# Optimization experiments

Hardware: AMD Instinct MI355X
Metric: run time of the kernel (lower is better)

The kernel has to match this reference:

```python
import jax, jax.numpy as jnp
import numpy as np

B, T, I, H, L = 32, 512, 1024, 1024, 2

def setup_inputs() -> dict:
    key = jax.random.key(0)
    ks = jax.random.split(key, 5)
    x = jax.random.normal(ks[0], (B, T, I), dtype=jnp.float32)
    # nn.Linear weight layout: [out_features, in_features] = [4H, in+H]
    scale0 = (6.0 / (4 * H + I + H)) ** 0.5  # xavier uniform bound
    scale1 = (6.0 / (4 * H + H + H)) ** 0.5
    W0 = jax.random.uniform(ks[1], (4 * H, I + H), minval=-scale0, maxval=scale0, dtype=jnp.float32)
    W1 = jax.random.uniform(ks[2], (4 * H, H + H), minval=-scale1, maxval=scale1, dtype=jnp.float32)
    # bias: zeros, with forget-gate slice (first H) set to 1, per reset_parameters
    b = jnp.zeros((4 * H,), dtype=jnp.float32).at[:H].set(1.0)
    return {"x": x, "W0": W0, "b0": b, "W1": W1, "b1": b}

def _cell(x_in, h_prev, c_prev, W, b):
    # combined:[B, in+H] @ W.T -> [B, 4H]
    gates = jnp.concatenate([x_in, h_prev], axis=1) @ W.T + b
    f, i, g, o = jnp.split(gates, 4, axis=1)
    f = jax.nn.sigmoid(f)
    i = jax.nn.sigmoid(i)
    g = jnp.tanh(g)
    o = jax.nn.sigmoid(o)
    c_next = f * c_prev + i * g
    h_next = o * jnp.tanh(c_next)
    return h_next, c_next

def reference(x, W0, b0, W1, b1):
    Ws = (W0, W1)
    bs = (b0, b1)
    x_t_major = jnp.transpose(x, (1, 0, 2))  # [T, B, I]
    h0 = jnp.zeros((L, B, H), dtype=x.dtype)
    c0 = jnp.zeros((L, B, H), dtype=x.dtype)

    def step(carry, x_t):
        h, c = carry
        inp = x_t
        hs, cs = [], []
        for l in range(L):
            h_new, c_new = _cell(inp, h[l], c[l], Ws[l], bs[l])
            hs.append(h_new)
            cs.append(c_new)
            inp = h_new  # dropout=0 -> identity between layers
        return (jnp.stack(hs), jnp.stack(cs)), inp

    (h_n, c_n), outs = jax.lax.scan(step, (h0, c0), x_t_major)
    outputs = jnp.transpose(outs, (1, 0, 2))  # batch_first
    return outputs, h_n, c_n
```

## Files before the change

### kernel.cpp

```cpp
#include <hip/hip_runtime.h>
#include <hip/hip_bf16.h>
#include <cstdint>
#include <cstddef>


typedef unsigned short ush;
typedef short bf16x8 __attribute__((ext_vector_type(8)));
typedef float f32x4 __attribute__((ext_vector_type(4)));
typedef int i32x4 __attribute__((ext_vector_type(4)));
typedef unsigned long long u64;

#define TT 512
#define NA 64
#define RING 8

__device__ __forceinline__ ush f2bf(float f) {
  __hip_bfloat16 h = __float2bfloat16(f);
  return *reinterpret_cast<ush*>(&h);
}
__device__ __forceinline__ float sigm(float x) { return 1.f / (1.f + __expf(-x)); }

__device__ __forceinline__ unsigned int aload(const unsigned int* p) {
  return __hip_atomic_load(p, __ATOMIC_RELAXED, __HIP_MEMORY_SCOPE_AGENT);
}
__device__ __forceinline__ void astore(unsigned int* p, unsigned int v) {
  __hip_atomic_store(p, v, __ATOMIC_RELAXED, __HIP_MEMORY_SCOPE_AGENT);
}
__device__ __forceinline__ float afload(const float* p) {
  return __hip_atomic_load(p, __ATOMIC_RELAXED, __HIP_MEMORY_SCOPE_AGENT);
}

__global__ __launch_bounds__(256) void cast_w1k(const float* __restrict__ W,
                                                ush* __restrict__ Wb, int off) {
  int j = blockIdx.x;
  int k = threadIdx.x * 4;
  float4 v = *(const float4*)(W + (size_t)j * 2048 + off + k);
  ushort4 o;
  o.x = f2bf(v.x); o.y = f2bf(v.y); o.z = f2bf(v.z); o.w = f2bf(v.w);
  *(ushort4*)(Wb + (size_t)j * 1024 + k) = o;
}

__global__ __launch_bounds__(256) void swzW(const float* __restrict__ W,
                                            ush* __restrict__ D, int coloff) {
  int n = blockIdx.x * 256 + threadIdx.x;
  int lane = n & 63, ch = (n >> 6) & 15, w = (n >> 10) & 7, i = n >> 13;
  int l15 = lane & 15, quad = lane >> 4, g = w & 3, kh = w >> 2;
  int row = g * 1024 + i * 16 + l15;
  int col = coloff + kh * 512 + ch * 32 + quad * 8;
  const float* src = W + (size_t)row * 2048 + col;
  float4 v0 = ((const float4*)src)[0];
  float4 v1 = ((const float4*)src)[1];
  ushort4 o0, o1;
  o0.x = f2bf(v0.x); o0.y = f2bf(v0.y); o0.z = f2bf(v0.z); o0.w = f2bf(v0.w);
  o1.x = f2bf(v1.x); o1.y = f2bf(v1.y); o1.z = f2bf(v1.z); o1.w = f2bf(v1.w);
  *(ushort4*)(D + (size_t)n * 8) = o0;
  *(ushort4*)(D + (size_t)n * 8 + 4) = o1;
}

__global__ __launch_bounds__(256) void swz1h(const float* __restrict__ W,
                                             ush* __restrict__ D) {
  int n = blockIdx.x * 256 + threadIdx.x;
  int lane = n & 63, ch = (n >> 6) & 7, w = (n >> 9) & 7, jb = n >> 12;
  int l15 = lane & 15, quad = lane >> 4, rh = w & 1, kq = w >> 1;
  int r32 = rh * 16 + l15;
  int row = (r32 >> 3) * 1024 + jb * 8 + (r32 & 7);
  int col = 1024 + kq * 256 + ch * 32 + quad * 8;
  const float* src = W + (size_t)row * 2048 + col;
  float4 v0 = ((const float4*)src)[0];
  float4 v1 = ((const float4*)src)[1];
  ushort4 o0, o1;
  o0.x = f2bf(v0.x); o0.y = f2bf(v0.y); o0.z = f2bf(v0.z); o0.w = f2bf(v0.w);
  o1.x = f2bf(v1.x); o1.y = f2bf(v1.y); o1.z = f2bf(v1.z); o1.w = f2bf(v1.w);
  *(ushort4*)(D + (size_t)n * 8) = o0;
  *(ushort4*)(D + (size_t)n * 8 + 4) = o1;
}

__global__ __launch_bounds__(256) void zeroreg(uint4* __restrict__ p) {
  p[blockIdx.x * 256 + threadIdx.x] = uint4{0, 0, 0, 0};
}

__global__ __launch_bounds__(256) void gemm128(
    const float* __restrict__ xA, const ush* __restrict__ Wb,
    const float* __restrict__ bias, float* __restrict__ G, int t0) {
  __shared__ ush As[128][88];
  __shared__ ush Bs[128][88];
  int tid = threadIdx.x;
  int bn = blockIdx.x, bm = blockIdx.y;
  int srow = tid >> 1;
  int shalf = (tid & 1) * 32;
  int lane = tid & 63, quad = lane >> 4, l15 = lane & 15;
  int w = tid >> 6;
  int m_base = (w >> 1) * 64, n_base = (w & 1) * 64;

  int r = bm * 128 + srow;
  const float* axf = xA + ((size_t)(r & 31) * TT + t0 + (r >> 5)) * 1024;
  const ush* wrow = Wb + (size_t)(bn * 128 + srow) * 1024;

  f32x4 acc[4][4];
#pragma unroll
  for (int i = 0; i < 4; ++i)
#pragma unroll
    for (int j = 0; j < 4; ++j) acc[i][j] = f32x4{0.f, 0.f, 0.f, 0.f};

  for (int k0 = 0; k0 < 1024; k0 += 64) {
    {
      const float* p = axf + k0 + shalf;
      ush* d = &As[srow][shalf];
#pragma unroll
      for (int s = 0; s < 8; ++s) {
        float4 v = ((const float4*)p)[s];
        ushort4 o;
        o.x = f2bf(v.x); o.y = f2bf(v.y); o.z = f2bf(v.z); o.w = f2bf(v.w);
        ((ushort4*)d)[s] = o;
      }
    }
    {
      const uint4* p = (const uint4*)(wrow + k0 + shalf);
      uint4* d = (uint4*)&Bs[srow][shalf];
#pragma unroll
      for (int s = 0; s < 4; ++s) d[s] = p[s];
    }
    __syncthreads();
#pragma unroll
    for (int kc = 0; kc < 2; ++kc) {
      bf16x8 af[4], bf_[4];
#pragma unroll
      for (int i = 0; i < 4; ++i)
        af[i] = *(const bf16x8*)&As[m_base + i * 16 + l15][kc * 32 + quad * 8];
#pragma unroll
      for (int j = 0; j < 4; ++j)
        bf_[j] = *(const bf16x8*)&Bs[n_base + j * 16 + l15][kc * 32 + quad * 8];
#pragma unroll
      for (int i = 0; i < 4; ++i)
#pragma unroll
        for (int j = 0; j < 4; ++j)
          acc[i][j] = __builtin_amdgcn_mfma_f32_16x16x32_bf16(af[i], bf_[j],
                                                              acc[i][j], 0, 0, 0);
    }
    __syncthreads();
  }

#pragma unroll
  for (int j = 0; j < 4; ++j) {
    int col = bn * 128 + n_base + j * 16 + l15;
    float bj = bias[col];
#pragma unroll
    for (int i = 0; i < 4; ++i) {
      int row = bm * 128 + m_base + i * 16 + quad * 4;
#pragma unroll
      for (int reg = 0; reg < 4; ++reg)
        G[(size_t)(row + reg) * 4096 + col] = acc[i][j][reg] + bj;
    }
  }
}

__global__ __launch_bounds__(512, 2) void lstm_persist(
    const float* __restrict__ G0, const ush* __restrict__ Wsw0,
    const ush* __restrict__ WswP, const ush* __restrict__ Wsw1h,
    const float* __restrict__ b1,
    ush* __restrict__ h0r, ush* __restrict__ h1r, float* __restrict__ Pr,
    unsigned int* __restrict__ flg,
    float* __restrict__ cst, float* __restrict__ OUT,
    float* __restrict__ hno, float* __restrict__ cno,
    int t0, int Tc, int last) {
  __shared__ ush hbuf[32768];
  __shared__ float pg[8][32][20];
  char* hb = (char*)hbuf;

  int tid = threadIdx.x;
  int bid = blockIdx.x;
  int w = tid >> 6, lane = tid & 63, quad = lane >> 4, l15 = lane & 15;
  unsigned int* prog0 = flg;
  unsigned int* prog1 = flg + 1024;
  unsigned int* progP = flg + 3072;

  if (bid < NA) {
    int c0 = bid * 16;
    const ush* wp = Wsw0 + ((size_t)bid * 8 + w) * 8192 + (size_t)lane * 8;
    bf16x8 wreg[16];
#pragma unroll
    for (int ch = 0; ch < 16; ++ch) wreg[ch] = *(const bf16x8*)(wp + ch * 512);
#pragma unroll
    for (int ch = 0; ch < 16; ++ch) asm volatile("" : "+v"(wreg[ch]));
    int b = tid >> 4, c = tid & 15;
    int ci = b * 1024 + c0 + c;
    float creg = (t0 > 0) ? cst[ci] : 0.f;
    int mPc = t0;
    int kbase = (w >> 2) * 1024 + quad * 16;
    int x0 = (l15 & 7) << 4;
    const char* a0p = hb + l15 * 2048;
    const char* a1p = hb + (16 + l15) * 2048;

    for (int s = 0; s < Tc; ++s) {
      int t = t0 + s;
      const float* grow = G0 + (size_t)(s * 32 + b) * 4096 + c0 + c;
      float g0v = grow[0], g1v = grow[1024], g2v = grow[2048], g3v = grow[3072];
      if (w == 0) {
        if ((int)aload(&prog0[lane * 16]) < t) {
          do { __builtin_amdgcn_s_sleep(1); } while ((int)aload(&prog0[lane * 16]) < t);
        }
        while (mPc < t - (RING - 1)) {
          int m = (int)aload(&progP[lane * 16]);
#pragma unroll
          for (int d = 1; d < 64; d <<= 1) m = min(m, __shfl_xor(m, d));
          mPc = m;
          if (mPc < t - (RING - 1)) __builtin_amdgcn_s_sleep(2);
        }
      }
      __syncthreads();
      {
        const char* src = (const char*)h0r + (size_t)((t - 1) & (RING - 1)) * 65536;
        i32x4 r_[8];
#pragma unroll
        for (int s2 = 0; s2 < 8; ++s2) {
          int gi = s2 * 512 + tid;
          asm volatile("global_load_dwordx4 %0, %1, off sc1"
                       : "=v"(r_[s2]) : "v"(src + (size_t)gi * 16));
        }
        asm volatile("s_waitcnt vmcnt(0)" ::: "memory");
        __builtin_amdgcn_sched_barrier(0);
#pragma unroll
        for (int s2 = 0; s2 < 8; ++s2) {
          int gi = s2 * 512 + tid;
          int r = gi >> 7, kb = (gi & 127) * 16;
          *(i32x4*)(hb + r * 2048 + (kb ^ ((r & 7) << 4))) = r_[s2];
        }
      }
      __syncthreads();
      f32x4 acc0 = {0.f, 0.f, 0.f, 0.f}, acc1 = {0.f, 0.f, 0.f, 0.f};
#pragma unroll
      for (int ch = 0; ch < 16; ++ch) {
        int kb = kbase + ch * 64;
        bf16x8 a0 = *(const bf16x8*)(a0p + (kb ^ x0));
        bf16x8 a1 = *(const bf16x8*)(a1p + (kb ^ x0));
        acc0 = __builtin_amdgcn_mfma_f32_16x16x32_bf16(a0, wreg[ch], acc0, 0, 0, 0);
        acc1 = __builtin_amdgcn_mfma_f32_16x16x32_bf16(a1, wreg[ch], acc1, 0, 0, 0);
      }
#pragma unroll
      for (int reg = 0; reg < 4; ++reg) {
        pg[w][quad * 4 + reg][l15] = acc0[reg];
        pg[w][16 + quad * 4 + reg][l15] = acc1[reg];
      }
      __syncthreads();
      float s0 = g0v + pg[0][b][c] + pg[4][b][c];
      float s1 = g1v + pg[1][b][c] + pg[5][b][c];
      float s2 = g2v + pg[2][b][c] + pg[6][b][c];
      float s3 = g3v + pg[3][b][c] + pg[7][b][c];
      float fg = sigm(s0), ig = sigm(s1), gv = tanhf(s2), og = sigm(s3);
      creg = fg * creg + ig * gv;
      float hnv = og * tanhf(creg);
      float ho = __shfl_xor(hnv, 1);
      unsigned int pk = (unsigned int)f2bf(hnv) | ((unsigned int)f2bf(ho) << 16);
      unsigned int pk2 = __shfl_xor(pk, 2);
      u64 d0 = (u64)pk | ((u64)pk2 << 32);
      u64 d1 = (u64)__shfl_xor((long long)d0, 4);
      if ((tid & 7) == 0) {
        i32x4 v;
        v.x = (int)d0; v.y = (int)(d0 >> 32);
        v.z = (int)d1; v.w = (int)(d1 >> 32);
        char* dp = (char*)(h0r + (size_t)(t & (RING - 1)) * 32768 +
                           (size_t)b * 1024 + c0 + c);
        asm volatile("global_store_dwordx4 %0, %1, off sc1"
                     :: "v"(dp), "v"(v) : "memory");
      }
      if (t == TT - 1) hno[ci] = hnv;
      asm volatile("s_waitcnt vmcnt(0)" ::: "memory");
      __syncthreads();
      if (tid == 0) astore(&prog0[bid * 16], (unsigned int)(t + 1));
    }
    cst[ci] = creg;
    if (last) cno[ci] = creg;
  } else if (bid < 2 * NA) {
    int p = bid - NA;
    int c0 = p * 16;
    const ush* wp = WswP + ((size_t)p * 8 + w) * 8192 + (size_t)lane * 8;
    bf16x8 wreg[16];
#pragma unroll
    for (int ch = 0; ch < 16; ++ch) wreg[ch] = *(const bf16x8*)(wp + ch * 512);
#pragma unroll
    for (int ch = 0; ch < 16; ++ch) asm volatile("" : "+v"(wreg[ch]));
    int b = tid >> 4, c = tid & 15;
    int m1c = t0;
    int kbase = (w >> 2) * 1024 + quad * 16;
    int x0 = (l15 & 7) << 4;
    const char* a0p = hb + l15 * 2048;
    const char* a1p = hb + (16 + l15) * 2048;

    for (int s = 0; s < Tc; ++s) {
      int t = t0 + s;
      if (w == 0) {
        if ((int)aload(&prog0[lane * 16]) < t + 1) {
          do { __builtin_amdgcn_s_sleep(1); } while ((int)aload(&prog0[lane * 16]) < t + 1);
        }
        while (m1c < t - (RING - 1)) {
          int m = (int)aload(&prog1[lane * 16]);
          m = min(m, (int)aload(&prog1[(64 + lane) * 16]));
#pragma unroll
          for (int d = 1; d < 64; d <<= 1) m = min(m, __shfl_xor(m, d));
          m1c = m;
          if (m1c < t - (RING - 1)) __builtin_amdgcn_s_sleep(2);
        }
      }
      __syncthreads();
      {
        const char* src = (const char*)h0r + (size_t)(t & (RING - 1)) * 65536;
        i32x4 r_[8];
#pragma unroll
        for (int s2 = 0; s2 < 8; ++s2) {
          int gi = s2 * 512 + tid;
          asm volatile("global_load_dwordx4 %0, %1, off sc1"
                       : "=v"(r_[s2]) : "v"(src + (size_t)gi * 16));
        }
        asm volatile("s_waitcnt vmcnt(0)" ::: "memory");
        __builtin_amdgcn_sched_barrier(0);
#pragma unroll
        for (int s2 = 0; s2 < 8; ++s2) {
          int gi = s2 * 512 + tid;
          int r = gi >> 7, kb = (gi & 127) * 16;
          *(i32x4*)(hb + r * 2048 + (kb ^ ((r & 7) << 4))) = r_[s2];
        }
      }
      __syncthreads();
      f32x4 acc0 = {0.f, 0.f, 0.f, 0.f}, acc1 = {0.f, 0.f, 0.f, 0.f};
#pragma unroll
      for (int ch = 0; ch < 16; ++ch) {
        int kb = kbase + ch * 64;
        bf16x8 a0 = *(const bf16x8*)(a0p + (kb ^ x0));
        bf16x8 a1 = *(const bf16x8*)(a1p + (kb ^ x0));
        acc0 = __builtin_amdgcn_mfma_f32_16x16x32_bf16(a0, wreg[ch], acc0, 0, 0, 0);
        acc1 = __builtin_amdgcn_mfma_f32_16x16x32_bf16(a1, wreg[ch], acc1, 0, 0, 0);
      }
#pragma unroll
      for (int reg = 0; reg < 4; ++reg) {
        pg[w][quad * 4 + reg][l15] = acc0[reg];
        pg[w][16 + quad * 4 + reg][l15] = acc1[reg];
      }
      __syncthreads();
      float s0 = pg[0][b][c] + pg[4][b][c];
      float s1 = pg[1][b][c] + pg[5][b][c];
      float s2 = pg[2][b][c] + pg[6][b][c];
      float s3 = pg[3][b][c] + pg[7][b][c];
      {
        i32x4 v;
        v.x = __float_as_int(s0); v.y = __float_as_int(s1);
        v.z = __float_as_int(s2); v.w = __float_as_int(s3);
        char* dp = (char*)Pr + (size_t)(t & (RING - 1)) * 524288 +
                   (size_t)(b * 1024 + c0 + c) * 16;
        asm volatile("global_store_dwordx4 %0, %1, off sc1"
                     :: "v"(dp), "v"(v) : "memory");
      }
      asm volatile("s_waitcnt vmcnt(0)" ::: "memory");
      __syncthreads();
      if (tid == 0) astore(&progP[p * 16], (unsigned int)(t + 1));
    }
  } else {
    int jb = bid - 2 * NA;
    int c0b = jb * 8;
    const ush* wp = Wsw1h + ((size_t)jb * 8 + w) * 4096 + (size_t)lane * 8;
    bf16x8 wreg[8];
#pragma unroll
    for (int ch = 0; ch < 8; ++ch) wreg[ch] = *(const bf16x8*)(wp + ch * 512);
#pragma unroll
    for (int ch = 0; ch < 8; ++ch) asm volatile("" : "+v"(wreg[ch]));
    bool pw = tid < 256;
    int b = tid >> 3, cc = tid & 7;
    int ci = b * 1024 + c0b + cc;
    float creg = 0.f;
    float biasr[4] = {0.f, 0.f, 0.f, 0.f};
    if (pw) {
      creg = (t0 > 0) ? cst[32768 + ci] : 0.f;
#pragma unroll
      for (int g = 0; g < 4; ++g) biasr[g] = b1[g * 1024 + c0b + cc];
    }
    int kq = w >> 1;
    int kbase = kq * 512 + quad * 16;
    int x0 = (l15 & 7) << 4;
    const char* a0p = hb + l15 * 2048;
    const char* a1p = hb + (16 + l15) * 2048;

    for (int s = 0; s < Tc; ++s) {
      int t = t0 + s;
      if (w == 0) {
        if ((int)aload(&progP[(jb >> 1) * 16]) < t + 1) {
          do { __builtin_amdgcn_s_sleep(1); } while ((int)aload(&progP[(jb >> 1) * 16]) < t + 1);
        }
      }
      __syncthreads();
      float pf[4] = {0.f, 0.f, 0.f, 0.f};
      if (pw) {
        const float* pp = (const float*)((const char*)Pr +
                          (size_t)(t & (RING - 1)) * 524288) +
                          (size_t)(b * 1024 + c0b + cc) * 4;
#pragma unroll
        for (int g = 0; g < 4; ++g) pf[g] = afload(pp + g);
      }
      if (w == 0) {
        while ((int)aload(&prog1[lane * 16]) < t ||
               (int)aload(&prog1[(64 + lane) * 16]) < t)
          __builtin_amdgcn_s_sleep(1);
      }
      __syncthreads();
      {
        const char* src = (const char*)h1r + (size_t)((t - 1) & (RING - 1)) * 65536;
        i32x4 r1_[8];
#pragma unroll
        for (int s2 = 0; s2 < 8; ++s2) {
          int gi = s2 * 512 + tid;
          asm volatile("global_load_dwordx4 %0, %1, off sc1"
                       : "=v"(r1_[s2]) : "v"(src + (size_t)gi * 16));
        }
        asm volatile("s_waitcnt vmcnt(0)" ::: "memory");
        __builtin_amdgcn_sched_barrier(0);
#pragma unroll
        for (int s2 = 0; s2 < 8; ++s2) {
          int gi = s2 * 512 + tid;
          int r = gi >> 7, kb = (gi & 127) * 16;
          *(i32x4*)(hb + r * 2048 + (kb ^ ((r & 7) << 4))) = r1_[s2];
        }
      }
      __syncthreads();
      f32x4 acc0 = {0.f, 0.f, 0.f, 0.f}, acc1 = {0.f, 0.f, 0.f, 0.f};
#pragma unroll
      for (int ch = 0; ch < 8; ++ch) {
        int kb = kbase + ch * 64;
        bf16x8 a0 = *(const bf16x8*)(a0p + (kb ^ x0));
        bf16x8 a1 = *(const bf16x8*)(a1p + (kb ^ x0));
        acc0 = __builtin_amdgcn_mfma_f32_16x16x32_bf16(a0, wreg[ch], acc0, 0, 0, 0);
        acc1 = __builtin_amdgcn_mfma_f32_16x16x32_bf16(a1, wreg[ch], acc1, 0, 0, 0);
      }
#pragma unroll
      for (int reg = 0; reg < 4; ++reg) {
        pg[w][quad * 4 + reg][l15] = acc0[reg];
        pg[w][16 + quad * 4 + reg][l15] = acc1[reg];
      }
      __syncthreads();
      float hnv = 0.f;
      if (pw) {
        float sg[4];
#pragma unroll
        for (int g = 0; g < 4; ++g) {
          int r = g * 8 + cc, rrh = r >> 4, ri = r & 15;
          sg[g] = biasr[g] + pf[g] + pg[rrh][b][ri] + pg[2 + rrh][b][ri] +
                  pg[4 + rrh][b][ri] + pg[6 + rrh][b][ri];
        }
        float fg = sigm(sg[0]), ig = sigm(sg[1]), gv = tanhf(sg[2]),
              og = sigm(sg[3]);
        creg = fg * creg + ig * gv;
        hnv = og * tanhf(creg);
        float ho = __shfl_xor(hnv, 1);
        unsigned int pk = (unsigned int)f2bf(hnv) | ((unsigned int)f2bf(ho) << 16);
        unsigned int pk2 = __shfl_xor(pk, 2);
        u64 d0 = (u64)pk | ((u64)pk2 << 32);
        u64 d1 = (u64)__shfl_xor((long long)d0, 4);
        if ((tid & 7) == 0) {
          i32x4 v;
          v.x = (int)d0; v.y = (int)(d0 >> 32);
          v.z = (int)d1; v.w = (int)(d1 >> 32);
          char* dp = (char*)(h1r + (size_t)(t & (RING - 1)) * 32768 +
                             (size_t)b * 1024 + c0b);
          asm volatile("global_store_dwordx4 %0, %1, off sc1"
                       :: "v"(dp), "v"(v) : "memory");
        }
      }
      asm volatile("s_waitcnt vmcnt(0)" ::: "memory");
      __syncthreads();
      if (tid == 0) astore(&prog1[jb * 16], (unsigned int)(t + 1));
      if (pw) {
        OUT[((size_t)b * TT + t) * 1024 + c0b + cc] = hnv;
        if (t == TT - 1) hno[32768 + ci] = hnv;
      }
    }
    if (pw) {
      cst[32768 + ci] = creg;
      if (last) cno[32768 + ci] = creg;
    }
  }
}

extern "C" void kernel_launch(void* const* d_in, const int* in_sizes, int n_in,
                              void* d_out, int out_size, void* d_ws, size_t ws_size,
                              hipStream_t stream) {
  const float* x = (const float*)d_in[0];
  const float* W0 = (const float*)d_in[1];
  const float* b0 = (const float*)d_in[2];
  const float* W1 = (const float*)d_in[3];
  const float* b1 = (const float*)d_in[4];
  float* OUT = (float*)d_out;

  int Tc = 4;
  {
    const int cand[8] = {512, 256, 128, 64, 32, 16, 8, 4};
    for (int i = 0; i < 8; ++i) {
      size_t need = 39075840ull + (size_t)cand[i] * 524288;
      if (need <= ws_size) { Tc = cand[i]; break; }
    }
  }
  char* ws = (char*)d_ws;
  ush* Wxb0 = (ush*)ws;
  ush* Wsw0 = (ush*)(ws + 8388608);
  ush* WswP = (ush*)(ws + 16777216);
  ush* Wsw1h = (ush*)(ws + 25165824);
  ush* h0r = (ush*)(ws + 33554432);
  ush* h1r = (ush*)(ws + 34078720);
  float* Pr = (float*)(ws + 34603008);
  unsigned int* flg = (unsigned int*)(ws + 38797312);
  float* cst = (float*)(ws + 38813696);
  float* G = (float*)(ws + 39075840);

  cast_w1k<<<4096, 256, 0, stream>>>(W0, Wxb0, 0);
  swzW<<<2048, 256, 0, stream>>>(W0, Wsw0, 1024);
  swzW<<<2048, 256, 0, stream>>>(W1, WswP, 0);
  swz1h<<<2048, 256, 0, stream>>>(W1, Wsw1h);
  zeroreg<<<1284, 256, 0, stream>>>((uint4*)(ws + 33554432));

  float* hnp = OUT + 16777216;
  float* cnp = OUT + 16777216 + 65536;
  dim3 ggrid(32, (unsigned)(Tc * 32 / 128));

  const int NCH = TT / Tc;
  for (int ch = 0; ch < NCH; ++ch) {
    int t0v = ch * Tc;
    int lastv = (ch == NCH - 1) ? 1 : 0;
    gemm128<<<ggrid, 256, 0, stream>>>(x, Wxb0, b0, G, t0v);
    void* pargs[16] = {(void*)&G,     (void*)&Wsw0, (void*)&WswP,
                       (void*)&Wsw1h, (void*)&b1,   (void*)&h0r,
                       (void*)&h1r,   (void*)&Pr,   (void*)&flg,
                       (void*)&cst,   (void*)&OUT,  (void*)&hnp,
                       (void*)&cnp,   (void*)&t0v,  (void*)&Tc,
                       (void*)&lastv};
    hipLaunchCooperativeKernel((void*)lstm_persist, dim3(4 * NA), dim3(512),
                               pargs, 0, stream);
  }
}
```

Before: 2.683 ms.

## Repartition layer-1 recurrent work to 32 blocks with full-K per wave

Layer-1 recurrent blocks drop from 128 to 32. Each wave now covers the full 1024-wide K dimension for 4 hidden columns across all four gates, so the cross-wave LDS reduction and its extra barrier are removed. Gate values are regrouped with in-register shuffles, and the P partials are read with two vector loads. This shrinks the grid and the number of progress flags polled. The cost is longer serial MFMA chains per wave and 32 weight vector registers per lane, which may cut occupancy and add per-step latency on the recurrent critical path.

```diff
diff --git a/kernel.cpp b/kernel.cpp
--- a/kernel.cpp
+++ b/kernel.cpp
@@ -8,6 +8,7 @@
 typedef short bf16x8 __attribute__((ext_vector_type(8)));
 typedef float f32x4 __attribute__((ext_vector_type(4)));
 typedef int i32x4 __attribute__((ext_vector_type(4)));
+typedef int i32x2 __attribute__((ext_vector_type(2)));
 typedef unsigned long long u64;
 
 #define TT 512
@@ -25,9 +26,6 @@
 }
 __device__ __forceinline__ void astore(unsigned int* p, unsigned int v) {
   __hip_atomic_store(p, v, __ATOMIC_RELAXED, __HIP_MEMORY_SCOPE_AGENT);
-}
-__device__ __forceinline__ float afload(const float* p) {
-  return __hip_atomic_load(p, __ATOMIC_RELAXED, __HIP_MEMORY_SCOPE_AGENT);
 }
 
 __global__ __launch_bounds__(256) void cast_w1k(const float* __restrict__ W,
@@ -57,14 +55,13 @@
   *(ushort4*)(D + (size_t)n * 8 + 4) = o1;
 }
 
-__global__ __launch_bounds__(256) void swz1h(const float* __restrict__ W,
+__global__ __launch_bounds__(256) void swz1n(const float* __restrict__ W,
                                              ush* __restrict__ D) {
   int n = blockIdx.x * 256 + threadIdx.x;
-  int lane = n & 63, ch = (n >> 6) & 7, w = (n >> 9) & 7, jb = n >> 12;
-  int l15 = lane & 15, quad = lane >> 4, rh = w & 1, kq = w >> 1;
-  int r32 = rh * 16 + l15;
-  int row = (r32 >> 3) * 1024 + jb * 8 + (r32 & 7);
-  int col = 1024 + kq * 256 + ch * 32 + quad * 8;
+  int lane = n & 63, ch = (n >> 6) & 31, w = (n >> 11) & 7, jb = n >> 14;
+  int l15 = lane & 15, quad = lane >> 4;
+  int row = (l15 >> 2) * 1024 + jb * 32 + w * 4 + (l15 & 3);
+  int col = 1024 + ch * 32 + quad * 8;
   const float* src = W + (size_t)row * 2048 + col;
   float4 v0 = ((const float4*)src)[0];
   float4 v1 = ((const float4*)src)[1];
@@ -156,7 +153,7 @@
 
 __global__ __launch_bounds__(512, 2) void lstm_persist(
     const float* __restrict__ G0, const ush* __restrict__ Wsw0,
-    const ush* __restrict__ WswP, const ush* __restrict__ Wsw1h,
+    const ush* __restrict__ WswP, const ush* __restrict__ Wsw1n,
     const float* __restrict__ b1,
     ush* __restrict__ h0r, ush* __restrict__ h1r, float* __restrict__ Pr,
     unsigned int* __restrict__ flg,
@@ -293,8 +290,7 @@
           do { __builtin_amdgcn_s_sleep(1); } while ((int)aload(&prog0[lane * 16]) < t + 1);
         }
         while (m1c < t - (RING - 1)) {
-          int m = (int)aload(&prog1[lane * 16]);
-          m = min(m, (int)aload(&prog1[(64 + lane) * 16]));
+          int m = (lane < 32) ? (int)aload(&prog1[lane * 16]) : 0x7fffffff;
 #pragma unroll
           for (int d = 1; d < 64; d <<= 1) m = min(m, __shfl_xor(m, d));
           m1c = m;
@@ -355,25 +351,22 @@
     }
   } else {
     int jb = bid - 2 * NA;
-    int c0b = jb * 8;
-    const ush* wp = Wsw1h + ((size_t)jb * 8 + w) * 4096 + (size_t)lane * 8;
-    bf16x8 wreg[8];
-#pragma unroll
-    for (int ch = 0; ch < 8; ++ch) wreg[ch] = *(const bf16x8*)(wp + ch * 512);
-#pragma unroll
-    for (int ch = 0; ch < 8; ++ch) asm volatile("" : "+v"(wreg[ch]));
-    bool pw = tid < 256;
-    int b = tid >> 3, cc = tid & 7;
-    int ci = b * 1024 + c0b + cc;
-    float creg = 0.f;
-    float biasr[4] = {0.f, 0.f, 0.f, 0.f};
-    if (pw) {
-      creg = (t0 > 0) ? cst[32768 + ci] : 0.f;
-#pragma unroll
-      for (int g = 0; g < 4; ++g) biasr[g] = b1[g * 1024 + c0b + cc];
-    }
-    int kq = w >> 1;
-    int kbase = kq * 512 + quad * 16;
+    int c0b = jb * 32;
+    const ush* wp = Wsw1n + (size_t)(jb * 8 + w) * 16384 + (size_t)lane * 8;
+    bf16x8 wreg[32];
+#pragma unroll
+    for (int ch = 0; ch < 32; ++ch) wreg[ch] = *(const bf16x8*)(wp + ch * 512);
+#pragma unroll
+    for (int ch = 0; ch < 32; ++ch) asm volatile("" : "+v"(wreg[ch]));
+    int cl = l15 & 3, bq = (l15 >> 2) & 3;
+    int col = c0b + w * 4 + cl;
+    int ba0 = quad * 4 + bq, ba1 = 16 + quad * 4 + bq;
+    int ci0 = ba0 * 1024 + col, ci1 = ba1 * 1024 + col;
+    float creg0 = (t0 > 0) ? cst[32768 + ci0] : 0.f;
+    float creg1 = (t0 > 0) ? cst[32768 + ci1] : 0.f;
+    float biasr[4];
+#pragma unroll
+    for (int g = 0; g < 4; ++g) biasr[g] = b1[g * 1024 + col];
     int x0 = (l15 & 7) << 4;
     const char* a0p = hb + l15 * 2048;
     const char* a1p = hb + (16 + l15) * 2048;
@@ -381,25 +374,24 @@
     for (int s = 0; s < Tc; ++s) {
       int t = t0 + s;
       if (w == 0) {
-        if ((int)aload(&progP[(jb >> 1) * 16]) < t + 1) {
-          do { __builtin_amdgcn_s_sleep(1); } while ((int)aload(&progP[(jb >> 1) * 16]) < t + 1);
-        }
-      }
-      __syncthreads();
-      float pf[4] = {0.f, 0.f, 0.f, 0.f};
-      if (pw) {
-        const float* pp = (const float*)((const char*)Pr +
-                          (size_t)(t & (RING - 1)) * 524288) +
-                          (size_t)(b * 1024 + c0b + cc) * 4;
-#pragma unroll
-        for (int g = 0; g < 4; ++g) pf[g] = afload(pp + g);
-      }
-      if (w == 0) {
-        while ((int)aload(&prog1[lane * 16]) < t ||
-               (int)aload(&prog1[(64 + lane) * 16]) < t)
-          __builtin_amdgcn_s_sleep(1);
-      }
-      __syncthreads();
+        if (lane < 2) {
+          while ((int)aload(&progP[(2 * jb + lane) * 16]) < t + 1)
+            __builtin_amdgcn_s_sleep(1);
+        }
+        if (lane < 32) {
+          while ((int)aload(&prog1[lane * 16]) < t)
+            __builtin_amdgcn_s_sleep(1);
+        }
+      }
+      __syncthreads();
+      i32x4 pf0, pf1;
+      {
+        const char* pps = (const char*)Pr + (size_t)(t & (RING - 1)) * 524288;
+        asm volatile("global_load_dwordx4 %0, %1, off sc1"
+                     : "=v"(pf0) : "v"(pps + (size_t)ci0 * 16));
+        asm volatile("global_load_dwordx4 %0, %1, off sc1"
+                     : "=v"(pf1) : "v"(pps + (size_t)ci1 * 16));
+      }
       {
         const char* src = (const char*)h1r + (size_t)((t - 1) & (RING - 1)) * 65536;
         i32x4 r1_[8];
@@ -421,59 +413,76 @@
       __syncthreads();
       f32x4 acc0 = {0.f, 0.f, 0.f, 0.f}, acc1 = {0.f, 0.f, 0.f, 0.f};
 #pragma unroll
-      for (int ch = 0; ch < 8; ++ch) {
-        int kb = kbase + ch * 64;
+      for (int ch = 0; ch < 32; ++ch) {
+        int kb = ch * 64 + quad * 16;
         bf16x8 a0 = *(const bf16x8*)(a0p + (kb ^ x0));
         bf16x8 a1 = *(const bf16x8*)(a1p + (kb ^ x0));
         acc0 = __builtin_amdgcn_mfma_f32_16x16x32_bf16(a0, wreg[ch], acc0, 0, 0, 0);
         acc1 = __builtin_amdgcn_mfma_f32_16x16x32_bf16(a1, wreg[ch], acc1, 0, 0, 0);
       }
-#pragma unroll
-      for (int reg = 0; reg < 4; ++reg) {
-        pg[w][quad * 4 + reg][l15] = acc0[reg];
-        pg[w][16 + quad * 4 + reg][l15] = acc1[reg];
-      }
-      __syncthreads();
-      float hnv = 0.f;
-      if (pw) {
-        float sg[4];
-#pragma unroll
-        for (int g = 0; g < 4; ++g) {
-          int r = g * 8 + cc, rrh = r >> 4, ri = r & 15;
-          sg[g] = biasr[g] + pf[g] + pg[rrh][b][ri] + pg[2 + rrh][b][ri] +
-                  pg[4 + rrh][b][ri] + pg[6 + rrh][b][ri];
-        }
-        float fg = sigm(sg[0]), ig = sigm(sg[1]), gv = tanhf(sg[2]),
-              og = sigm(sg[3]);
-        creg = fg * creg + ig * gv;
-        hnv = og * tanhf(creg);
-        float ho = __shfl_xor(hnv, 1);
-        unsigned int pk = (unsigned int)f2bf(hnv) | ((unsigned int)f2bf(ho) << 16);
-        unsigned int pk2 = __shfl_xor(pk, 2);
-        u64 d0 = (u64)pk | ((u64)pk2 << 32);
-        u64 d1 = (u64)__shfl_xor((long long)d0, 4);
-        if ((tid & 7) == 0) {
-          i32x4 v;
-          v.x = (int)d0; v.y = (int)(d0 >> 32);
-          v.z = (int)d1; v.w = (int)(d1 >> 32);
-          char* dp = (char*)(h1r + (size_t)(t & (RING - 1)) * 32768 +
-                             (size_t)b * 1024 + c0b);
-          asm volatile("global_store_dwordx4 %0, %1, off sc1"
-                       :: "v"(dp), "v"(v) : "memory");
-        }
+      {
+        float t0_, t1_, r0_, r1_;
+        if ((bq & 1) == 0) { t0_ = acc0[1]; t1_ = acc0[3]; }
+        else               { t0_ = acc0[0]; t1_ = acc0[2]; }
+        r0_ = __shfl_xor(t0_, 4); r1_ = __shfl_xor(t1_, 4);
+        if ((bq & 1) == 0) { acc0[1] = r0_; acc0[3] = r1_; }
+        else               { acc0[0] = r0_; acc0[2] = r1_; }
+        if ((bq & 2) == 0) { t0_ = acc0[2]; t1_ = acc0[3]; }
+        else               { t0_ = acc0[0]; t1_ = acc0[1]; }
+        r0_ = __shfl_xor(t0_, 8); r1_ = __shfl_xor(t1_, 8);
+        if ((bq & 2) == 0) { acc0[2] = r0_; acc0[3] = r1_; }
+        else               { acc0[0] = r0_; acc0[1] = r1_; }
+        if ((bq & 1) == 0) { t0_ = acc1[1]; t1_ = acc1[3]; }
+        else               { t0_ = acc1[0]; t1_ = acc1[2]; }
+        r0_ = __shfl_xor(t0_, 4); r1_ = __shfl_xor(t1_, 4);
+        if ((bq & 1) == 0) { acc1[1] = r0_; acc1[3] = r1_; }
+        else               { acc1[0] = r0_; acc1[2] = r1_; }
+        if ((bq & 2) == 0) { t0_ = acc1[2]; t1_ = acc1[3]; }
+        else               { t0_ = acc1[0]; t1_ = acc1[1]; }
+        r0_ = __shfl_xor(t0_, 8); r1_ = __shfl_xor(t1_, 8);
+        if ((bq & 2) == 0) { acc1[2] = r0_; acc1[3] = r1_; }
+        else               { acc1[0] = r0_; acc1[1] = r1_; }
+      }
+      float s00 = acc0[0] + __int_as_float(pf0[0]) + biasr[0];
+      float s01 = acc0[1] + __int_as_float(pf0[1]) + biasr[1];
+      float s02 = acc0[2] + __int_as_float(pf0[2]) + biasr[2];
+      float s03 = acc0[3] + __int_as_float(pf0[3]) + biasr[3];
+      float s10 = acc1[0] + __int_as_float(pf1[0]) + biasr[0];
+      float s11 = acc1[1] + __int_as_float(pf1[1]) + biasr[1];
+      float s12 = acc1[2] + __int_as_float(pf1[2]) + biasr[2];
+      float s13 = acc1[3] + __int_as_float(pf1[3]) + biasr[3];
+      float fg0 = sigm(s00), ig0 = sigm(s01), gg0 = tanhf(s02), og0 = sigm(s03);
+      float fg1 = sigm(s10), ig1 = sigm(s11), gg1 = tanhf(s12), og1 = sigm(s13);
+      creg0 = fg0 * creg0 + ig0 * gg0;
+      creg1 = fg1 * creg1 + ig1 * gg1;
+      float h0v = og0 * tanhf(creg0);
+      float h1v = og1 * tanhf(creg1);
+      unsigned pkA = (unsigned)f2bf(h0v) | ((unsigned)f2bf(__shfl_xor(h0v, 1)) << 16);
+      unsigned pkAb = __shfl_xor(pkA, 2);
+      unsigned pkB = (unsigned)f2bf(h1v) | ((unsigned)f2bf(__shfl_xor(h1v, 1)) << 16);
+      unsigned pkBb = __shfl_xor(pkB, 2);
+      if (cl == 0) {
+        i32x2 vA; vA[0] = (int)pkA; vA[1] = (int)pkAb;
+        char* dpA = (char*)(h1r + (size_t)(t & (RING - 1)) * 32768 +
+                            (size_t)ba0 * 1024 + col);
+        asm volatile("global_store_dwordx2 %0, %1, off sc1"
+                     :: "v"(dpA), "v"(vA) : "memory");
+        i32x2 vB; vB[0] = (int)pkB; vB[1] = (int)pkBb;
+        char* dpB = (char*)(h1r + (size_t)(t & (RING - 1)) * 32768 +
+                            (size_t)ba1 * 1024 + col);
+        asm volatile("global_store_dwordx2 %0, %1, off sc1"
+                     :: "v"(dpB), "v"(vB) : "memory");
       }
       asm volatile("s_waitcnt vmcnt(0)" ::: "memory");
       __syncthreads();
       if (tid == 0) astore(&prog1[jb * 16], (unsigned int)(t + 1));
-      if (pw) {
-        OUT[((size_t)b * TT + t) * 1024 + c0b + cc] = hnv;
-        if (t == TT - 1) hno[32768 + ci] = hnv;
-      }
-    }
-    if (pw) {
-      cst[32768 + ci] = creg;
-      if (last) cno[32768 + ci] = creg;
-    }
+      OUT[((size_t)ba0 * TT + t) * 1024 + col] = h0v;
+      OUT[((size_t)ba1 * TT + t) * 1024 + col] = h1v;
+      if (t == TT - 1) { hno[32768 + ci0] = h0v; hno[32768 + ci1] = h1v; }
+    }
+    cst[32768 + ci0] = creg0;
+    cst[32768 + ci1] = creg1;
+    if (last) { cno[32768 + ci0] = creg0; cno[32768 + ci1] = creg1; }
   }
 }
 
@@ -499,7 +508,7 @@
   ush* Wxb0 = (ush*)ws;
   ush* Wsw0 = (ush*)(ws + 8388608);
   ush* WswP = (ush*)(ws + 16777216);
-  ush* Wsw1h = (ush*)(ws + 25165824);
+  ush* Wsw1n = (ush*)(ws + 25165824);
   ush* h0r = (ush*)(ws + 33554432);
   ush* h1r = (ush*)(ws + 34078720);
   float* Pr = (float*)(ws + 34603008);
@@ -510,7 +519,7 @@
   cast_w1k<<<4096, 256, 0, stream>>>(W0, Wxb0, 0);
   swzW<<<2048, 256, 0, stream>>>(W0, Wsw0, 1024);
   swzW<<<2048, 256, 0, stream>>>(W1, WswP, 0);
-  swz1h<<<2048, 256, 0, stream>>>(W1, Wsw1h);
+  swz1n<<<2048, 256, 0, stream>>>(W1, Wsw1n);
   zeroreg<<<1284, 256, 0, stream>>>((uint4*)(ws + 33554432));
 
   float* hnp = OUT + 16777216;
@@ -523,12 +532,12 @@
     int lastv = (ch == NCH - 1) ? 1 : 0;
     gemm128<<<ggrid, 256, 0, stream>>>(x, Wxb0, b0, G, t0v);
     void* pargs[16] = {(void*)&G,     (void*)&Wsw0, (void*)&WswP,
-                       (void*)&Wsw1h, (void*)&b1,   (void*)&h0r,
+                       (void*)&Wsw1n, (void*)&b1,   (void*)&h0r,
                        (void*)&h1r,   (void*)&Pr,   (void*)&flg,
                        (void*)&cst,   (void*)&OUT,  (void*)&hnp,
                        (void*)&cnp,   (void*)&t0v,  (void*)&Tc,
                        (void*)&lastv};
-    hipLaunchCooperativeKernel((void*)lstm_persist, dim3(4 * NA), dim3(512),
+    hipLaunchCooperativeKernel((void*)lstm_persist, dim3(2 * NA + 32), dim3(512),
                                pargs, 0, stream);
   }
 }
```

Measured after the change: 3.334 ms. 24.2% more time.
